# Optimization experiments

Hardware: AMD Instinct MI355X
Metric: run time of the kernel (lower is better)

Reference implementation:

```python
import jax, jax.numpy as jnp
import numpy as np

WS = (7, 7, 7)
DIM = 96
HEADS = 3
NW = 64          # windows per image (mask batch)
BW = 512         # B_ = total windows = 8 images * 64 windows
N = WS[0] * WS[1] * WS[2]  # 343


def _rel_pos_index(ws):
    # Faithful reproduction of the torch buffer (including its multipliers).
    coords = np.stack(np.meshgrid(np.arange(ws[0]), np.arange(ws[1]), np.arange(ws[2]), indexing='ij'))
    cf = coords.reshape(3, -1)                      # [3, N]
    rc = cf[:, :, None] - cf[:, None, :]            # [3, N, N]
    rc = rc.transpose(1, 2, 0).astype(np.int32)     # [N, N, 3]
    rc[:, :, 0] += ws[0] - 1
    rc[:, :, 1] += ws[1] - 1
    rc[:, :, 2] += ws[2] - 1
    rc[:, :, 0] *= 3 * ws[1] - 1
    rc[:, :, 1] *= 2 * ws[1] - 1
    return rc.sum(-1)                               # [N, N]


def setup_inputs() -> dict:
    key = jax.random.key(0)
    ks = jax.random.split(key, 8)
    table_len = (2 * WS[0] - 1) * (2 * WS[1] - 1) * (2 * WS[2] - 1)  # 2197
    x = jax.random.normal(ks[0], (BW, N, DIM), dtype=jnp.float32)
    # shift-window additive mask: 0 where allowed, -100 where masked
    mask = jnp.where(jax.random.uniform(ks[1], (NW, N, N)) < 0.9, 0.0, -100.0).astype(jnp.float32)
    Wqkv = jax.random.normal(ks[2], (3 * DIM, DIM), dtype=jnp.float32) * 0.02
    bqkv = jnp.zeros((3 * DIM,), dtype=jnp.float32)
    Wproj = jax.random.normal(ks[3], (DIM, DIM), dtype=jnp.float32) * 0.02
    bproj = jnp.zeros((DIM,), dtype=jnp.float32)
    logit_scale = jnp.full((HEADS, 1, 1), np.log(10.0), dtype=jnp.float32)
    bias_table = jax.random.normal(ks[4], (table_len, HEADS), dtype=jnp.float32) * 0.02
    rpi = jnp.asarray(_rel_pos_index(WS))           # [N, N] int32
    return {"x": x, "mask": mask, "Wqkv": Wqkv, "bqkv": bqkv,
            "Wproj": Wproj, "bproj": bproj, "logit_scale": logit_scale,
            "bias_table": bias_table, "rpi": rpi}


def reference(x, mask, Wqkv, bqkv, Wproj, bproj, logit_scale, bias_table, rpi):
    B_, Nn, C = x.shape
    H = HEADS
    hd = C // H
    qkv = x @ Wqkv.T + bqkv                          # [B_, N, 3C]
    qkv = qkv.reshape(B_, Nn, 3, H, hd).transpose(2, 0, 3, 1, 4)  # [3, B_, H, N, hd]
    q, k, v = qkv[0], qkv[1], qkv[2]
    # cosine attention: L2-normalize q and k (torch F.normalize, eps=1e-12)
    qn = q / jnp.maximum(jnp.linalg.norm(q, axis=-1, keepdims=True), 1e-12)
    kn = k / jnp.maximum(jnp.linalg.norm(k, axis=-1, keepdims=True), 1e-12)
    attn = jnp.einsum('bhnd,bhmd->bhnm', qn, kn)     # [B_, H, N, N]
    scale = jnp.exp(jnp.minimum(logit_scale, jnp.log(jnp.float32(100.0))))  # [H,1,1]
    attn = attn * scale[None]
    rel_bias = bias_table[rpi.reshape(-1)].reshape(Nn, Nn, H).transpose(2, 0, 1)  # [H, N, N]
    attn = attn + rel_bias[None]
    nW = mask.shape[0]
    attn = attn.reshape(B_ // nW, nW, H, Nn, Nn) + mask[None, :, None]
    attn = attn.reshape(B_, H, Nn, Nn)
    attn = jax.nn.softmax(attn, axis=-1)
    out = jnp.einsum('bhnm,bhmd->bhnd', attn, v)     # [B_, H, N, hd]
    out = out.transpose(0, 2, 1, 3).reshape(B_, Nn, C)
    return out @ Wproj.T + bproj
```

## Files before the change

### kernel.cpp

```cpp
#include <hip/hip_runtime.h>

typedef __attribute__((ext_vector_type(8))) _Float16 half8;
typedef __attribute__((ext_vector_type(4))) _Float16 half4;
typedef __attribute__((ext_vector_type(4))) float f32x4;

__device__ __forceinline__ _Float16 f2h(float f) { return (_Float16)f; }

#define LOG100 4.605170185988091f
#define NEGBIG -30000.0f

__global__ void k_maskb(const float* __restrict__ mask, unsigned char* __restrict__ mb) {
  int tid = blockIdx.x * 256 + threadIdx.x;
  if (tid >= 64 * 484 * 64) return;
  int lane = tid & 63, idx = tid >> 6;
  int kt = idx % 22, t2 = idx / 22;
  int qt = t2 % 22, w = t2 / 22;
  int R = qt * 16 + (lane & 15), col0 = kt * 16 + (lane >> 4) * 4;
  unsigned bits = 0;
#pragma unroll
  for (int rr = 0; rr < 4; rr++) {
    int col = col0 + rr;
    bool pass = true;
    if (R < 343 && col < 343) pass = mask[((size_t)w * 343 + R) * 343 + col] > -50.f;
    bits |= (pass ? 1u : 0u) << rr;
  }
  mb[tid] = (unsigned char)bits;
}

__global__ void k_biasf(const int* __restrict__ rpi, const float* __restrict__ table,
                        _Float16* __restrict__ bf) {
  int tid = blockIdx.x * 256 + threadIdx.x;
  if (tid >= 3 * 484 * 64) return;
  int lane = tid & 63, idx = tid >> 6;
  int kt = idx % 22, t2 = idx / 22;
  int qt = t2 % 22, h = t2 / 22;
  int R = qt * 16 + (lane & 15), col0 = kt * 16 + (lane >> 4) * 4;
  half4 o;
#pragma unroll
  for (int rr = 0; rr < 4; rr++) {
    int col = col0 + rr;
    float b = (R < 343 && col < 343) ? table[rpi[R * 343 + col] * 3 + h] : NEGBIG;
    o[rr] = f2h(b);
  }
  reinterpret_cast<half4*>(bf)[tid] = o;
}

__global__ __launch_bounds__(1024, 1) void k_qkv(
    const float* __restrict__ x, const float* __restrict__ Wqkv,
    const float* __restrict__ bqkv, const float* __restrict__ ls,
    _Float16* __restrict__ q_ws, _Float16* __restrict__ k_ws, _Float16* __restrict__ v_ws) {
  __shared__ alignas(16) _Float16 Wl[288 * 104];
  const int tid = threadIdx.x;
  for (int i = tid; i < 6912; i += 1024) {
    f32x4 w4 = reinterpret_cast<const f32x4*>(Wqkv)[i];
    int f = i * 4, row = f / 96, col = f - row * 96;
    _Float16* dst = &Wl[row * 104 + col];
    dst[0] = f2h(w4[0]); dst[1] = f2h(w4[1]); dst[2] = f2h(w4[2]); dst[3] = f2h(w4[3]);
  }
  __syncthreads();
  const int lane = tid & 63, wv = tid >> 6;
  const int ln15 = lane & 15, quad = lane >> 4;
  const int rowbase = blockIdx.x * 256 + wv * 16;
  const int arow = rowbase + ln15;

  half8 afr[3];
#pragma unroll
  for (int kt = 0; kt < 3; kt++) {
    const float* xp = x + (size_t)arow * 96 + kt * 32 + quad * 8;
    f32x4 a0 = *reinterpret_cast<const f32x4*>(xp);
    f32x4 a1 = *reinterpret_cast<const f32x4*>(xp + 4);
    half8 a;
    a[0] = f2h(a0[0]); a[1] = f2h(a0[1]); a[2] = f2h(a0[2]); a[3] = f2h(a0[3]);
    a[4] = f2h(a1[0]); a[5] = f2h(a1[1]); a[6] = f2h(a1[2]); a[7] = f2h(a1[3]);
    afr[kt] = a;
  }

  int Bb[4], Nn[4];
#pragma unroll
  for (int rr = 0; rr < 4; rr++) {
    int R = rowbase + quad * 4 + rr;
    Bb[rr] = R / 343;
    Nn[rr] = R - Bb[rr] * 343;
  }

  auto ctile = [&](int nt) -> f32x4 {
    f32x4 c = {0.f, 0.f, 0.f, 0.f};
#pragma unroll
    for (int kt = 0; kt < 3; kt++) {
      half8 b = *reinterpret_cast<const half8*>(&Wl[(nt * 16 + ln15) * 104 + kt * 32 + quad * 8]);
      c = __builtin_amdgcn_mfma_f32_16x16x32_f16(afr[kt], b, c, 0, 0, 0);
    }
    return c;
  };

#pragma unroll
  for (int h = 0; h < 3; h++) {
    float sc = __expf(fminf(ls[h], LOG100));
    {
      f32x4 c0 = ctile(2 * h), c1 = ctile(2 * h + 1);
      float b0 = bqkv[32 * h + ln15], b1 = bqkv[32 * h + 16 + ln15];
#pragma unroll
      for (int rr = 0; rr < 4; rr++) { c0[rr] += b0; c1[rr] += b1; }
#pragma unroll
      for (int rr = 0; rr < 4; rr++) {
        float s2 = c0[rr] * c0[rr] + c1[rr] * c1[rr];
        s2 += __shfl_xor(s2, 1); s2 += __shfl_xor(s2, 2);
        s2 += __shfl_xor(s2, 4); s2 += __shfl_xor(s2, 8);
        float inv = sc / fmaxf(sqrtf(s2), 1e-12f);
        size_t base = ((size_t)(Bb[rr] * 3 + h) * 343 + Nn[rr]) * 32;
        q_ws[base + ln15] = f2h(c0[rr] * inv);
        q_ws[base + 16 + ln15] = f2h(c1[rr] * inv);
      }
    }
    {
      f32x4 c0 = ctile(6 + 2 * h), c1 = ctile(7 + 2 * h);
      float b0 = bqkv[96 + 32 * h + ln15], b1 = bqkv[96 + 32 * h + 16 + ln15];
#pragma unroll
      for (int rr = 0; rr < 4; rr++) { c0[rr] += b0; c1[rr] += b1; }
#pragma unroll
      for (int rr = 0; rr < 4; rr++) {
        float s2 = c0[rr] * c0[rr] + c1[rr] * c1[rr];
        s2 += __shfl_xor(s2, 1); s2 += __shfl_xor(s2, 2);
        s2 += __shfl_xor(s2, 4); s2 += __shfl_xor(s2, 8);
        float inv = 1.0f / fmaxf(sqrtf(s2), 1e-12f);
        size_t base = ((size_t)(Bb[rr] * 3 + h) * 343 + Nn[rr]) * 32;
        k_ws[base + ln15] = f2h(c0[rr] * inv);
        k_ws[base + 16 + ln15] = f2h(c1[rr] * inv);
      }
    }
    {
      f32x4 c0 = ctile(12 + 2 * h), c1 = ctile(13 + 2 * h);
      float b0 = bqkv[192 + 32 * h + ln15], b1 = bqkv[192 + 32 * h + 16 + ln15];
#pragma unroll
      for (int rr = 0; rr < 4; rr++) {
        size_t base = ((size_t)(Bb[rr] * 3 + h) * 343 + Nn[rr]) * 32;
        v_ws[base + ln15] = f2h(c0[rr] + b0);
        v_ws[base + 16 + ln15] = f2h(c1[rr] + b1);
      }
    }
  }
}

#define KSTR 40
#define VSTR 352
#define PSTR 40
__global__ __launch_bounds__(384, 3) void k_attn(
    const _Float16* __restrict__ q_ws, const _Float16* __restrict__ k_ws,
    const _Float16* __restrict__ v_ws, const half4* __restrict__ bfrag,
    const unsigned char* __restrict__ mb, _Float16* __restrict__ a_ws) {
  __shared__ alignas(16) _Float16 Kl[344 * KSTR];
  __shared__ alignas(16) _Float16 Vt[32 * VSTR];
  __shared__ alignas(16) _Float16 Pl[6][16 * PSTR];
  const int blk = blockIdx.x;
  const int b = blk / 3, h = blk - b * 3, w = b & 63;
  const size_t slice = (size_t)(b * 3 + h) * 343 * 32;
  const _Float16* qb = q_ws + slice;
  const _Float16* kb = k_ws + slice;
  const _Float16* vb = v_ws + slice;
  const int tid = threadIdx.x, lane = tid & 63, wv = tid >> 6;
  const int ln15 = lane & 15, quad = lane >> 4;

  for (int i = tid; i < 344 * 4; i += 384) {
    int t = i >> 2, c4 = i & 3;
    half8 kv;
    if (t < 343) kv = *reinterpret_cast<const half8*>(kb + t * 32 + c4 * 8);
    else kv = (half8)(_Float16)0.f;
    *reinterpret_cast<half8*>(&Kl[t * KSTR + c4 * 8]) = kv;
  }
  for (int i = tid; i < 1372; i += 384) {
    int n = i >> 2, c4 = i & 3;
    half8 vv = *reinterpret_cast<const half8*>(vb + n * 32 + c4 * 8);
#pragma unroll
    for (int j = 0; j < 8; j++) Vt[(c4 * 8 + j) * VSTR + n] = vv[j];
  }
  for (int i = tid; i < 288; i += 384) {
    int d = i / 9, cc = i - d * 9;
    Vt[d * VSTR + 343 + cc] = (_Float16)0.f;
  }
  __syncthreads();

  _Float16* Pw = Pl[wv];
  const half4* bfh = bfrag + (size_t)h * 484 * 64;
  const unsigned char* mbw = mb + (size_t)w * 484 * 64;

#pragma unroll 1
  for (int qt = wv; qt < 22; qt += 6) {
    const int qbase = qt * 16;
    half8 aq = *reinterpret_cast<const half8*>(qb + (size_t)(qbase + ln15) * 32 + quad * 8);
    const half4* bq = bfh + (size_t)qt * 22 * 64 + lane;
    const unsigned char* mq = mbw + (size_t)qt * 22 * 64 + lane;

    f32x4 o0 = {0.f, 0.f, 0.f, 0.f}, o1 = {0.f, 0.f, 0.f, 0.f};
    float l = 0.f;

    half4 b4a = bq[0], b4b = bq[64];
    unsigned mva = mq[0], mvb = mq[64];

#pragma unroll 1
    for (int kc = 0; kc < 11; kc++) {
      int r0 = kc * 32 + ln15;
      int r1 = r0 + 16;
      r1 = (r1 > 343) ? 343 : r1;
      half8 ak0 = *reinterpret_cast<const half8*>(&Kl[r0 * KSTR + quad * 8]);
      half8 ak1 = *reinterpret_cast<const half8*>(&Kl[r1 * KSTR + quad * 8]);
      f32x4 z = {0.f, 0.f, 0.f, 0.f};
      f32x4 s0 = __builtin_amdgcn_mfma_f32_16x16x32_f16(ak0, aq, z, 0, 0, 0);
      f32x4 s1 = __builtin_amdgcn_mfma_f32_16x16x32_f16(ak1, aq, z, 0, 0, 0);

      half4 nb4a = b4a, nb4b = b4b;
      unsigned nmva = mva, nmvb = mvb;
      if (kc < 10) {
        nb4a = bq[(2 * kc + 2) * 64]; nb4b = bq[(2 * kc + 3) * 64];
        nmva = mq[(2 * kc + 2) * 64]; nmvb = mq[(2 * kc + 3) * 64];
      }

      float p0[4], p1[4];
#pragma unroll
      for (int rr = 0; rr < 4; rr++) {
        float sv0 = s0[rr] + (float)b4a[rr] + (((mva >> rr) & 1u) ? 0.f : -100.f);
        float sv1 = s1[rr] + (float)b4b[rr] + (((mvb >> rr) & 1u) ? 0.f : -100.f);
        p0[rr] = __expf(sv0);
        p1[rr] = __expf(sv1);
        l += p0[rr] + p1[rr];
      }
      half4 ph0, ph1;
#pragma unroll
      for (int rr = 0; rr < 4; rr++) { ph0[rr] = f2h(p0[rr]); ph1[rr] = f2h(p1[rr]); }
      *reinterpret_cast<half4*>(&Pw[ln15 * PSTR + quad * 4]) = ph0;
      *reinterpret_cast<half4*>(&Pw[ln15 * PSTR + 16 + quad * 4]) = ph1;

      asm volatile("s_waitcnt lgkmcnt(0)" ::: "memory");

      half8 pb = *reinterpret_cast<const half8*>(&Pw[ln15 * PSTR + quad * 8]);
      half8 v0 = *reinterpret_cast<const half8*>(&Vt[ln15 * VSTR + kc * 32 + quad * 8]);
      half8 v1 = *reinterpret_cast<const half8*>(&Vt[(16 + ln15) * VSTR + kc * 32 + quad * 8]);
      o0 = __builtin_amdgcn_mfma_f32_16x16x32_f16(v0, pb, o0, 0, 0, 0);
      o1 = __builtin_amdgcn_mfma_f32_16x16x32_f16(v1, pb, o1, 0, 0, 0);

      asm volatile("" ::: "memory");

      b4a = nb4a; b4b = nb4b; mva = nmva; mvb = nmvb;
    }

    l += __shfl_xor(l, 16);
    l += __shfl_xor(l, 32);

    const int R = qbase + ln15;
    if (R < 343) {
      float inv = 1.0f / l;
      size_t obase = ((size_t)b * 343 + R) * 96 + h * 32;
      half4 w0, w1;
#pragma unroll
      for (int rr = 0; rr < 4; rr++) {
        w0[rr] = f2h(o0[rr] * inv);
        w1[rr] = f2h(o1[rr] * inv);
      }
      *reinterpret_cast<half4*>(a_ws + obase + quad * 4) = w0;
      *reinterpret_cast<half4*>(a_ws + obase + 16 + quad * 4) = w1;
    }
  }
}

__global__ __launch_bounds__(1024, 1) void k_proj(
    const _Float16* __restrict__ a_ws, const float* __restrict__ Wproj,
    const float* __restrict__ bproj, float* __restrict__ out) {
  __shared__ alignas(16) _Float16 Wl[96 * 104];
  const int tid = threadIdx.x;
  for (int i = tid; i < 2304; i += 1024) {
    f32x4 w4 = reinterpret_cast<const f32x4*>(Wproj)[i];
    int f = i * 4, row = f / 96, col = f - row * 96;
    _Float16* dst = &Wl[row * 104 + col];
    dst[0] = f2h(w4[0]); dst[1] = f2h(w4[1]); dst[2] = f2h(w4[2]); dst[3] = f2h(w4[3]);
  }
  __syncthreads();
  const int lane = tid & 63, wv = tid >> 6;
  const int ln15 = lane & 15, quad = lane >> 4;
  const int rowbase = blockIdx.x * 256 + wv * 16;
  half8 afr[3];
#pragma unroll
  for (int kt = 0; kt < 3; kt++) {
    afr[kt] = *reinterpret_cast<const half8*>(a_ws + (size_t)(rowbase + ln15) * 96 + kt * 32 + quad * 8);
  }
#pragma unroll
  for (int nt = 0; nt < 6; nt++) {
    f32x4 c = {0.f, 0.f, 0.f, 0.f};
#pragma unroll
    for (int kt = 0; kt < 3; kt++) {
      half8 bfr = *reinterpret_cast<const half8*>(&Wl[(nt * 16 + ln15) * 104 + kt * 32 + quad * 8]);
      c = __builtin_amdgcn_mfma_f32_16x16x32_f16(afr[kt], bfr, c, 0, 0, 0);
    }
    float bb = bproj[nt * 16 + ln15];
#pragma unroll
    for (int rr = 0; rr < 4; rr++) {
      int R = rowbase + quad * 4 + rr;
      out[(size_t)R * 96 + nt * 16 + ln15] = c[rr] + bb;
    }
  }
}

extern "C" void kernel_launch(void* const* d_in, const int* in_sizes, int n_in,
                              void* d_out, int out_size, void* d_ws, size_t ws_size,
                              hipStream_t stream) {
  const float* x     = (const float*)d_in[0];
  const float* mask  = (const float*)d_in[1];
  const float* Wqkv  = (const float*)d_in[2];
  const float* bqkv  = (const float*)d_in[3];
  const float* Wproj = (const float*)d_in[4];
  const float* bproj = (const float*)d_in[5];
  const float* ls    = (const float*)d_in[6];
  const float* btab  = (const float*)d_in[7];
  const int*   rpi   = (const int*)d_in[8];
  float* out = (float*)d_out;

  char* ws = (char*)d_ws;
  _Float16* q_ws = (_Float16*)(ws);
  _Float16* k_ws = (_Float16*)(ws + 33718272);
  _Float16* v_ws = (_Float16*)(ws + 67436544);
  _Float16* a_ws = (_Float16*)(ws + 101154816);
  _Float16* bfrag = (_Float16*)(ws + 134873088);
  unsigned char* mbf = (unsigned char*)(ws + 135616512);

  hipLaunchKernelGGL(k_maskb, dim3((64 * 484 * 64 + 255) / 256), dim3(256), 0, stream, mask, mbf);
  hipLaunchKernelGGL(k_biasf, dim3((3 * 484 * 64 + 255) / 256), dim3(256), 0, stream, rpi, btab, bfrag);
  hipLaunchKernelGGL(k_qkv, dim3(686), dim3(1024), 0, stream, x, Wqkv, bqkv, ls, q_ws, k_ws, v_ws);
  hipLaunchKernelGGL(k_attn, dim3(1536), dim3(384), 0, stream, q_ws, k_ws, v_ws,
                     (const half4*)bfrag, mbf, a_ws);
  hipLaunchKernelGGL(k_proj, dim3(686), dim3(1024), 0, stream, a_ws, Wproj, bproj, out);
}
```

Measured before the change: 347.4 us.

## Transpose P in registers via permlane swaps and switch softmax to exp2

The attention inner loop no longer stages the probability tile through per-wave LDS with a waitcnt. The fp16 P fragments are instead rearranged into the MFMA B-operand layout with permlane32/permlane16 swap instructions. The log2(e) factor is folded into the q scale and the relative-position bias, which is now stored as fp32, so the exponential becomes a raw exp2. Masked entries are zeroed with a select instead of adding -100, the row sums use fdot2 on the packed halves, and the occupancy hint rises from 3 to 4 blocks. The risks are a larger bias buffer to read and small numeric differences from round-toward-zero packing and from dropping exp(-100) terms.

```diff
diff --git a/kernel.cpp b/kernel.cpp
--- a/kernel.cpp
+++ b/kernel.cpp
@@ -3,11 +3,15 @@
 typedef __attribute__((ext_vector_type(8))) _Float16 half8;
 typedef __attribute__((ext_vector_type(4))) _Float16 half4;
 typedef __attribute__((ext_vector_type(4))) float f32x4;
+typedef __attribute__((ext_vector_type(2))) unsigned int uint2v;
+typedef __attribute__((ext_vector_type(4))) unsigned int uint4v;
 
 __device__ __forceinline__ _Float16 f2h(float f) { return (_Float16)f; }
 
 #define LOG100 4.605170185988091f
-#define NEGBIG -30000.0f
+#define LOG2E 1.44269504088896f
+#define MASKNEG (-144.269504089f)
+#define PADNEG (-100000.0f)
 
 __global__ void k_maskb(const float* __restrict__ mask, unsigned char* __restrict__ mb) {
   int tid = blockIdx.x * 256 + threadIdx.x;
@@ -28,21 +32,20 @@
 }
 
 __global__ void k_biasf(const int* __restrict__ rpi, const float* __restrict__ table,
-                        _Float16* __restrict__ bf) {
+                        float* __restrict__ bf) {
   int tid = blockIdx.x * 256 + threadIdx.x;
   if (tid >= 3 * 484 * 64) return;
   int lane = tid & 63, idx = tid >> 6;
   int kt = idx % 22, t2 = idx / 22;
   int qt = t2 % 22, h = t2 / 22;
   int R = qt * 16 + (lane & 15), col0 = kt * 16 + (lane >> 4) * 4;
-  half4 o;
+  f32x4 o;
 #pragma unroll
   for (int rr = 0; rr < 4; rr++) {
     int col = col0 + rr;
-    float b = (R < 343 && col < 343) ? table[rpi[R * 343 + col] * 3 + h] : NEGBIG;
-    o[rr] = f2h(b);
-  }
-  reinterpret_cast<half4*>(bf)[tid] = o;
+    o[rr] = (R < 343 && col < 343) ? table[rpi[R * 343 + col] * 3 + h] * LOG2E : PADNEG;
+  }
+  reinterpret_cast<f32x4*>(bf)[tid] = o;
 }
 
 __global__ __launch_bounds__(1024, 1) void k_qkv(
@@ -95,7 +98,7 @@
 
 #pragma unroll
   for (int h = 0; h < 3; h++) {
-    float sc = __expf(fminf(ls[h], LOG100));
+    float sc = __expf(fminf(ls[h], LOG100)) * LOG2E;
     {
       f32x4 c0 = ctile(2 * h), c1 = ctile(2 * h + 1);
       float b0 = bqkv[32 * h + ln15], b1 = bqkv[32 * h + 16 + ln15];
@@ -142,15 +145,13 @@
 }
 
 #define KSTR 40
-#define VSTR 352
-#define PSTR 40
-__global__ __launch_bounds__(384, 3) void k_attn(
+#define VSTR 360
+__global__ __launch_bounds__(384, 4) void k_attn(
     const _Float16* __restrict__ q_ws, const _Float16* __restrict__ k_ws,
-    const _Float16* __restrict__ v_ws, const half4* __restrict__ bfrag,
+    const _Float16* __restrict__ v_ws, const float* __restrict__ bfrag,
     const unsigned char* __restrict__ mb, _Float16* __restrict__ a_ws) {
   __shared__ alignas(16) _Float16 Kl[344 * KSTR];
   __shared__ alignas(16) _Float16 Vt[32 * VSTR];
-  __shared__ alignas(16) _Float16 Pl[6][16 * PSTR];
   const int blk = blockIdx.x;
   const int b = blk / 3, h = blk - b * 3, w = b & 63;
   const size_t slice = (size_t)(b * 3 + h) * 343 * 32;
@@ -179,22 +180,23 @@
   }
   __syncthreads();
 
-  _Float16* Pw = Pl[wv];
-  const half4* bfh = bfrag + (size_t)h * 484 * 64;
+  const float* bfh = bfrag + (size_t)h * 484 * 64 * 4;
   const unsigned char* mbw = mb + (size_t)w * 484 * 64;
+  const auto kOnes = __builtin_amdgcn_cvt_pkrtz(1.f, 1.f);
 
 #pragma unroll 1
   for (int qt = wv; qt < 22; qt += 6) {
     const int qbase = qt * 16;
     half8 aq = *reinterpret_cast<const half8*>(qb + (size_t)(qbase + ln15) * 32 + quad * 8);
-    const half4* bq = bfh + (size_t)qt * 22 * 64 + lane;
+    const f32x4* bq = reinterpret_cast<const f32x4*>(bfh) + (size_t)qt * 22 * 64 + lane;
     const unsigned char* mq = mbw + (size_t)qt * 22 * 64 + lane;
 
     f32x4 o0 = {0.f, 0.f, 0.f, 0.f}, o1 = {0.f, 0.f, 0.f, 0.f};
-    float l = 0.f;
-
-    half4 b4a = bq[0], b4b = bq[64];
+    float l0 = 0.f, l1 = 0.f;
+
+    f32x4 ba = bq[0], bb = bq[64];
     unsigned mva = mq[0], mvb = mq[64];
+    bq += 128; mq += 128;
 
 #pragma unroll 1
     for (int kc = 0; kc < 11; kc++) {
@@ -207,41 +209,51 @@
       f32x4 s0 = __builtin_amdgcn_mfma_f32_16x16x32_f16(ak0, aq, z, 0, 0, 0);
       f32x4 s1 = __builtin_amdgcn_mfma_f32_16x16x32_f16(ak1, aq, z, 0, 0, 0);
 
-      half4 nb4a = b4a, nb4b = b4b;
+      f32x4 nba = ba, nbb = bb;
       unsigned nmva = mva, nmvb = mvb;
       if (kc < 10) {
-        nb4a = bq[(2 * kc + 2) * 64]; nb4b = bq[(2 * kc + 3) * 64];
-        nmva = mq[(2 * kc + 2) * 64]; nmvb = mq[(2 * kc + 3) * 64];
+        nba = bq[0]; nbb = bq[64];
+        nmva = mq[0]; nmvb = mq[64];
+        bq += 128; mq += 128;
       }
 
       float p0[4], p1[4];
 #pragma unroll
       for (int rr = 0; rr < 4; rr++) {
-        float sv0 = s0[rr] + (float)b4a[rr] + (((mva >> rr) & 1u) ? 0.f : -100.f);
-        float sv1 = s1[rr] + (float)b4b[rr] + (((mvb >> rr) & 1u) ? 0.f : -100.f);
-        p0[rr] = __expf(sv0);
-        p1[rr] = __expf(sv1);
-        l += p0[rr] + p1[rr];
-      }
-      half4 ph0, ph1;
-#pragma unroll
-      for (int rr = 0; rr < 4; rr++) { ph0[rr] = f2h(p0[rr]); ph1[rr] = f2h(p1[rr]); }
-      *reinterpret_cast<half4*>(&Pw[ln15 * PSTR + quad * 4]) = ph0;
-      *reinterpret_cast<half4*>(&Pw[ln15 * PSTR + 16 + quad * 4]) = ph1;
-
-      asm volatile("s_waitcnt lgkmcnt(0)" ::: "memory");
-
-      half8 pb = *reinterpret_cast<const half8*>(&Pw[ln15 * PSTR + quad * 8]);
+        float e0 = __builtin_amdgcn_exp2f(s0[rr] + ba[rr]);
+        float e1 = __builtin_amdgcn_exp2f(s1[rr] + bb[rr]);
+        p0[rr] = ((mva >> rr) & 1u) ? e0 : 0.f;
+        p1[rr] = ((mvb >> rr) & 1u) ? e1 : 0.f;
+      }
+      auto w00 = __builtin_amdgcn_cvt_pkrtz(p0[0], p0[1]);
+      auto w01 = __builtin_amdgcn_cvt_pkrtz(p0[2], p0[3]);
+      auto w10 = __builtin_amdgcn_cvt_pkrtz(p1[0], p1[1]);
+      auto w11 = __builtin_amdgcn_cvt_pkrtz(p1[2], p1[3]);
+      l0 = __builtin_amdgcn_fdot2(w00, kOnes, l0, false);
+      l1 = __builtin_amdgcn_fdot2(w01, kOnes, l1, false);
+      l0 = __builtin_amdgcn_fdot2(w10, kOnes, l0, false);
+      l1 = __builtin_amdgcn_fdot2(w11, kOnes, l1, false);
+
+      unsigned a0 = __builtin_bit_cast(unsigned int, w00);
+      unsigned a1 = __builtin_bit_cast(unsigned int, w01);
+      unsigned b0 = __builtin_bit_cast(unsigned int, w10);
+      unsigned b1 = __builtin_bit_cast(unsigned int, w11);
+      uint2v r32a = __builtin_amdgcn_permlane32_swap(a0, b0, false, false);
+      uint2v r32b = __builtin_amdgcn_permlane32_swap(a1, b1, false, false);
+      uint2v r16a = __builtin_amdgcn_permlane16_swap(r32a[0], r32a[1], false, false);
+      uint2v r16b = __builtin_amdgcn_permlane16_swap(r32b[0], r32b[1], false, false);
+      uint4v pw = {r16a[0], r16b[0], r16a[1], r16b[1]};
+      half8 pb = __builtin_bit_cast(half8, pw);
+
       half8 v0 = *reinterpret_cast<const half8*>(&Vt[ln15 * VSTR + kc * 32 + quad * 8]);
       half8 v1 = *reinterpret_cast<const half8*>(&Vt[(16 + ln15) * VSTR + kc * 32 + quad * 8]);
       o0 = __builtin_amdgcn_mfma_f32_16x16x32_f16(v0, pb, o0, 0, 0, 0);
       o1 = __builtin_amdgcn_mfma_f32_16x16x32_f16(v1, pb, o1, 0, 0, 0);
 
-      asm volatile("" ::: "memory");
-
-      b4a = nb4a; b4b = nb4b; mva = nmva; mvb = nmvb;
-    }
-
+      ba = nba; bb = nbb; mva = nmva; mvb = nmvb;
+    }
+
+    float l = l0 + l1;
     l += __shfl_xor(l, 16);
     l += __shfl_xor(l, 32);
 
@@ -317,13 +329,13 @@
   _Float16* k_ws = (_Float16*)(ws + 33718272);
   _Float16* v_ws = (_Float16*)(ws + 67436544);
   _Float16* a_ws = (_Float16*)(ws + 101154816);
-  _Float16* bfrag = (_Float16*)(ws + 134873088);
-  unsigned char* mbf = (unsigned char*)(ws + 135616512);
+  float* bfrag = (float*)(ws + 134873088);
+  unsigned char* mbf = (unsigned char*)(ws + 136359936);
 
   hipLaunchKernelGGL(k_maskb, dim3((64 * 484 * 64 + 255) / 256), dim3(256), 0, stream, mask, mbf);
   hipLaunchKernelGGL(k_biasf, dim3((3 * 484 * 64 + 255) / 256), dim3(256), 0, stream, rpi, btab, bfrag);
   hipLaunchKernelGGL(k_qkv, dim3(686), dim3(1024), 0, stream, x, Wqkv, bqkv, ls, q_ws, k_ws, v_ws);
   hipLaunchKernelGGL(k_attn, dim3(1536), dim3(384), 0, stream, q_ws, k_ws, v_ws,
-                     (const half4*)bfrag, mbf, a_ws);
+                     bfrag, mbf, a_ws);
   hipLaunchKernelGGL(k_proj, dim3(686), dim3(1024), 0, stream, a_ws, Wproj, bproj, out);
 }
```

Result: faster. 310.7 us (-10.6%).
